# Kernel tuning notes

Measured on AMD Instinct MI355X. Metric: run time of the kernel, lower is better.

The kernel has to match this reference:

```python
import jax, jax.numpy as jnp
import numpy as np

EPS = 1e-6

def _rmsnorm(x, w):
    # Qwen3RMSNorm over last dim, computed in fp32
    var = jnp.mean(jnp.square(x), axis=-1, keepdims=True)
    return x * jax.lax.rsqrt(var + EPS) * w

def setup_inputs() -> dict:
    key = jax.random.key(0)
    ks = jax.random.split(key, 8)
    NSEQ, IN_DIM, H, G, D, SINK = 16384, 4096, 8, 4, 16, 16
    s = 0.02
    return {
        "hidden_states": jax.random.normal(ks[0], (1, NSEQ, IN_DIM), jnp.float32),
        "q_w": jax.random.normal(ks[1], (H * G * D, IN_DIM), jnp.float32) * s,
        "q_b": jax.random.normal(ks[2], (H * G * D,), jnp.float32) * s,
        "k_w": jax.random.normal(ks[3], (H * D, IN_DIM), jnp.float32) * s,
        "q_norm_w": jnp.ones((D,), jnp.float32),
        "k_norm_w": jnp.ones((D,), jnp.float32),
        "k_base": jax.random.normal(ks[4], (H, 1, SINK, D), jnp.float32) * s,
        "b": jax.random.normal(ks[5], (H, 1, G), jnp.float32) * s,
    }

def reference(hidden_states, q_w, q_b, k_w, q_norm_w, k_norm_w, k_base, b):
    H, _, SINK, D = k_base.shape
    G = b.shape[-1]
    d = jnp.sqrt(jnp.asarray(D, hidden_states.dtype))
    h = hidden_states[0]                                   # [n, in_dim]
    n = h.shape[0]
    # projections + RMSNorm
    q = _rmsnorm((h @ q_w.T + q_b).reshape(n, H, G, D), q_norm_w)   # [n,H,G,D]
    k = _rmsnorm((h @ k_w.T).reshape(n, H, D), k_norm_w)            # [n,H,D]
    # logit: per-token key against its own group queries + learned bias
    logit = jnp.einsum('nhd,nhgd->hng', k, q) / d + b               # [H,n,G]
    # logit_base: learned sink keys against queries
    logit_base = jnp.einsum('hsd,nhgd->hnsg', k_base[:, 0], q) / d  # [H,n,S,G]
    # sigmoid-difference gate, summed over sink tokens
    denom = 1.0 + jnp.sum(jnp.exp(logit_base - logit[:, :, None, :]), axis=2)  # [H,n,G]
    score = jnp.mean(1.0 / denom, axis=-1)                          # [H,n]
    return score[None]                                              # [1,H,n]
```

## Files before the change

kernel.cpp:

```cpp
#include <hip/hip_runtime.h>
#include <hip/hip_bf16.h>

typedef __attribute__((ext_vector_type(8))) short bf16x8;
typedef __attribute__((ext_vector_type(4))) float f32x4;
typedef unsigned short u16;

constexpr int NSEQ = 16384;
constexpr int KD   = 4096;
constexpr int NQ   = 512;
constexpr int NCOL = 640;
constexpr int BM   = 64;
constexpr int BK   = 64;
constexpr int NKSTEP = KD / BK;
constexpr int CHUNKS_PER_TILE = NCOL * BK * 2 / 16;
constexpr int TOTAL_CHUNKS = CHUNKS_PER_TILE * NKSTEP;

__device__ __forceinline__ unsigned bf_round(float x) {
    unsigned u = __builtin_bit_cast(unsigned, x);
    unsigned r = u + 0x7FFFu + ((u >> 16) & 1u);
    return r >> 16;
}
__device__ __forceinline__ unsigned pk2(float lo, float hi) {
    return bf_round(lo) | (bf_round(hi) << 16);
}

__global__ __launch_bounds__(256) void wconv_kernel(
    const float* __restrict__ qw, const float* __restrict__ kw,
    u16* __restrict__ Wst)
{
    int cg = blockIdx.x * 256 + threadIdx.x;
    int kk = cg / CHUNKS_PER_TILE;
    int c  = cg - kk * CHUNKS_PER_TILE;
    int n  = c >> 3;
    int s  = c & 7;
    int k0 = kk * BK + ((s ^ (n & 7)) << 3);
    const float* src = (n < NQ) ? (qw + (size_t)n * KD + k0)
                                : (kw + (size_t)(n - NQ) * KD + k0);
    float4 v0 = *(const float4*)(src);
    float4 v1 = *(const float4*)(src + 4);
    int4 o;
    o.x = (int)pk2(v0.x, v0.y);
    o.y = (int)pk2(v0.z, v0.w);
    o.z = (int)pk2(v1.x, v1.y);
    o.w = (int)pk2(v1.z, v1.w);
    *(int4*)(Wst + (size_t)cg * 8) = o;
}

__global__ __launch_bounds__(512, 2) void gemm_kernel(
    const float* __restrict__ hid, const u16* __restrict__ Wst,
    float* __restrict__ P)
{
    __shared__ char smem[NCOL * BK * 2 + BM * BK * 2];
    char* sB = smem;
    char* sA = smem + NCOL * BK * 2;

    const int t    = threadIdx.x;
    const int lane = t & 63;
    const int wid  = t >> 6;
    const int wm   = wid >> 2;
    const int wq   = wid & 3;
    const int row0 = blockIdx.x * BM;

    f32x4 acc[2][10] = {};

    const int ar = t >> 3;
    const int as = t & 7;
    const float* gA = hid + (size_t)(row0 + ar) * KD + (as << 3);
    char* aDst = sA + ar * (BK * 2) + ((as * 16) ^ ((ar & 7) << 4));

    const int bn  = lane & 15;
    const int kb8 = (lane >> 4) << 3;
    const int swz = (bn & 7) << 4;

    char* bLdsBase = sB + wid * 64 * 16;

    float4 v0 = *(const float4*)(gA);
    float4 v1 = *(const float4*)(gA + 4);

    for (int kk = 0; kk < NKSTEP; ++kk) {
        const u16* tile = Wst + (size_t)kk * (CHUNKS_PER_TILE * 8);
        #pragma unroll
        for (int it = 0; it < 10; ++it) {
            __builtin_amdgcn_global_load_lds(
                (const __attribute__((address_space(1))) void*)(tile + (size_t)(it * 512 + t) * 8),
                (__attribute__((address_space(3))) void*)(bLdsBase + it * 512 * 16),
                16, 0, 0);
        }
        int4 ap;
        ap.x = (int)pk2(v0.x, v0.y);
        ap.y = (int)pk2(v0.z, v0.w);
        ap.z = (int)pk2(v1.x, v1.y);
        ap.w = (int)pk2(v1.z, v1.w);
        *(int4*)aDst = ap;

        __syncthreads();

        if (kk + 1 < NKSTEP) {
            v0 = *(const float4*)(gA + (kk + 1) * BK);
            v1 = *(const float4*)(gA + (kk + 1) * BK + 4);
        }

        #pragma unroll
        for (int ks = 0; ks < 2; ++ks) {
            const int k2 = ks * 64 + kb8 * 2;
            const int ko = k2 ^ swz;
            bf16x8 a0 = *(const bf16x8*)(sA + (wm * 32 + bn) * 128 + ko);
            bf16x8 a1 = *(const bf16x8*)(sA + (wm * 32 + 16 + bn) * 128 + ko);
            bf16x8 bf[10];
            #pragma unroll
            for (int f = 0; f < 10; ++f) {
                const int nn = wq * 160 + f * 16 + bn;
                bf[f] = *(const bf16x8*)(sB + nn * 128 + ko);
            }
            #pragma unroll
            for (int f = 0; f < 10; ++f) {
                acc[0][f] = __builtin_amdgcn_mfma_f32_16x16x32_bf16(a0, bf[f], acc[0][f], 0, 0, 0);
                acc[1][f] = __builtin_amdgcn_mfma_f32_16x16x32_bf16(a1, bf[f], acc[1][f], 0, 0, 0);
            }
        }
        __syncthreads();
    }

    const int crow = (lane >> 4) << 2;
    const int ccol = lane & 15;
    #pragma unroll
    for (int mi = 0; mi < 2; ++mi) {
        #pragma unroll
        for (int f = 0; f < 10; ++f) {
            #pragma unroll
            for (int j = 0; j < 4; ++j) {
                int r  = row0 + wm * 32 + mi * 16 + crow + j;
                int cc = wq * 160 + f * 16 + ccol;
                P[(size_t)r * NCOL + cc] = acc[mi][f][j];
            }
        }
    }
}

__global__ __launch_bounds__(256) void gate_kernel(
    const float* __restrict__ P, const float* __restrict__ qb,
    const float* __restrict__ qnw, const float* __restrict__ knw,
    const float* __restrict__ kbase, const float* __restrict__ bb,
    float* __restrict__ out)
{
    __shared__ float skb[8 * 16 * 16];
    __shared__ float sqb[512];
    __shared__ float sb[32];
    __shared__ float snw[32];

    int tid = threadIdx.x;
    for (int i = tid; i < 2048; i += 256) skb[i] = kbase[i];
    for (int i = tid; i < 512;  i += 256) sqb[i] = qb[i];
    if (tid < 32) sb[tid] = bb[tid];
    if (tid < 16) snw[tid] = qnw[tid];
    else if (tid < 32) snw[tid] = knw[tid - 16];
    __syncthreads();

    int gid = blockIdx.x * 256 + tid;
    int tok = gid >> 5;
    int hh  = (gid >> 2) & 7;
    int g   = gid & 3;

    const float* prow = P + (size_t)tok * NCOL;
    const int qoff = (hh * 4 + g) * 16;

    float q[16];
    float ss = 0.f;
    {
        const float4* qp = (const float4*)(prow + qoff);
        const float4* bp = (const float4*)(sqb + qoff);
        #pragma unroll
        for (int i = 0; i < 4; ++i) {
            float4 v = qp[i], b4 = bp[i];
            q[4*i+0] = v.x + b4.x; q[4*i+1] = v.y + b4.y;
            q[4*i+2] = v.z + b4.z; q[4*i+3] = v.w + b4.w;
        }
        #pragma unroll
        for (int d = 0; d < 16; ++d) ss += q[d] * q[d];
    }
    float rq = rsqrtf(ss * (1.f / 16.f) + 1e-6f);
    #pragma unroll
    for (int d = 0; d < 16; ++d) q[d] *= rq * snw[d];

    float k[16];
    float sk = 0.f;
    {
        const float4* kp = (const float4*)(prow + NQ + hh * 16);
        #pragma unroll
        for (int i = 0; i < 4; ++i) {
            float4 v = kp[i];
            k[4*i+0] = v.x; k[4*i+1] = v.y; k[4*i+2] = v.z; k[4*i+3] = v.w;
        }
        #pragma unroll
        for (int d = 0; d < 16; ++d) sk += k[d] * k[d];
    }
    float rk = rsqrtf(sk * (1.f / 16.f) + 1e-6f);

    float logit = 0.f;
    #pragma unroll
    for (int d = 0; d < 16; ++d) logit += (k[d] * rk * snw[16 + d]) * q[d];
    logit = logit * 0.25f + sb[hh * 4 + g];

    float accum = 0.f;
    const float* kbh = skb + hh * 256;
    #pragma unroll
    for (int s = 0; s < 16; ++s) {
        float lb = 0.f;
        #pragma unroll
        for (int d = 0; d < 16; ++d) lb += kbh[s * 16 + d] * q[d];
        accum += __expf(lb * 0.25f - logit);
    }
    float r = 1.f / (1.f + accum);

    r += __shfl_xor(r, 1);
    r += __shfl_xor(r, 2);
    if (g == 0) out[(size_t)hh * NSEQ + tok] = r * 0.25f;
}

extern "C" void kernel_launch(void* const* d_in, const int* in_sizes, int n_in,
                              void* d_out, int out_size, void* d_ws, size_t ws_size,
                              hipStream_t stream)
{
    const float* hid = (const float*)d_in[0];
    const float* qw  = (const float*)d_in[1];
    const float* qb  = (const float*)d_in[2];
    const float* kw  = (const float*)d_in[3];
    const float* qnw = (const float*)d_in[4];
    const float* knw = (const float*)d_in[5];
    const float* kb  = (const float*)d_in[6];
    const float* bb  = (const float*)d_in[7];
    float* out = (float*)d_out;

    u16*   Wst = (u16*)d_ws;
    float* P   = (float*)((char*)d_ws + (size_t)NCOL * KD * 2);

    wconv_kernel<<<TOTAL_CHUNKS / 256, 256, 0, stream>>>(qw, kw, Wst);
    gemm_kernel<<<NSEQ / BM, 512, 0, stream>>>(hid, Wst, P);
    gate_kernel<<<NSEQ * 32 / 256, 256, 0, stream>>>(P, qb, qnw, knw, kb, bb, out);
}
```

Measured before the change: 190.7 us.

## Split-K GEMM with double-buffered LDS, larger M tile, and bf16 partial outputs

Restructures the projection GEMM into a two-way split over K, with 256 blocks of 128 rows each. Each block double-buffers LDS tiles with BK=32 and prefetches the next weight tile and A rows, so global loads overlap the MFMA work and one barrier per step is removed. The partial results are stored as bf16 into two buffers, and the gate kernel sums them, which halves the P write and read traffic per partial. In exchange the extra rounding of partials to bf16 adds precision risk, and the block count now fits only one wave of CUs.

```diff
diff --git a/kernel.cpp b/kernel.cpp
--- a/kernel.cpp
+++ b/kernel.cpp
@@ -9,11 +9,15 @@
 constexpr int KD   = 4096;
 constexpr int NQ   = 512;
 constexpr int NCOL = 640;
-constexpr int BM   = 64;
-constexpr int BK   = 64;
-constexpr int NKSTEP = KD / BK;
+constexpr int BM   = 128;
+constexpr int BK   = 32;
+constexpr int KHALF = 2048;
+constexpr int NKS  = KHALF / BK;
 constexpr int CHUNKS_PER_TILE = NCOL * BK * 2 / 16;
-constexpr int TOTAL_CHUNKS = CHUNKS_PER_TILE * NKSTEP;
+constexpr int NTILES = KD / BK;
+constexpr int TOTAL_CHUNKS = CHUNKS_PER_TILE * NTILES;
+constexpr int TILE_U16 = CHUNKS_PER_TILE * 8;
+constexpr int BUF_BYTES = 49152;
 
 __device__ __forceinline__ unsigned bf_round(float x) {
     unsigned u = __builtin_bit_cast(unsigned, x);
@@ -23,6 +27,9 @@
 __device__ __forceinline__ unsigned pk2(float lo, float hi) {
     return bf_round(lo) | (bf_round(hi) << 16);
 }
+__device__ __forceinline__ float bfu(unsigned u) {
+    return __builtin_bit_cast(float, u << 16);
+}
 
 __global__ __launch_bounds__(256) void wconv_kernel(
     const float* __restrict__ qw, const float* __restrict__ kw,
@@ -31,9 +38,9 @@
     int cg = blockIdx.x * 256 + threadIdx.x;
     int kk = cg / CHUNKS_PER_TILE;
     int c  = cg - kk * CHUNKS_PER_TILE;
-    int n  = c >> 3;
-    int s  = c & 7;
-    int k0 = kk * BK + ((s ^ (n & 7)) << 3);
+    int n  = c >> 2;
+    int s  = c & 3;
+    int k0 = kk * BK + ((s ^ (n & 3)) << 3);
     const float* src = (n < NQ) ? (qw + (size_t)n * KD + k0)
                                 : (kw + (size_t)(n - NQ) * KD + k0);
     float4 v0 = *(const float4*)(src);
@@ -48,97 +55,132 @@
 
 __global__ __launch_bounds__(512, 2) void gemm_kernel(
     const float* __restrict__ hid, const u16* __restrict__ Wst,
-    float* __restrict__ P)
-{
-    __shared__ char smem[NCOL * BK * 2 + BM * BK * 2];
-    char* sB = smem;
-    char* sA = smem + NCOL * BK * 2;
+    u16* __restrict__ P0, u16* __restrict__ P1)
+{
+    __shared__ char smem[2 * BUF_BYTES];
 
     const int t    = threadIdx.x;
     const int lane = t & 63;
     const int wid  = t >> 6;
     const int wm   = wid >> 2;
     const int wq   = wid & 3;
-    const int row0 = blockIdx.x * BM;
-
-    f32x4 acc[2][10] = {};
-
-    const int ar = t >> 3;
-    const int as = t & 7;
-    const float* gA = hid + (size_t)(row0 + ar) * KD + (as << 3);
-    char* aDst = sA + ar * (BK * 2) + ((as * 16) ^ ((ar & 7) << 4));
-
-    const int bn  = lane & 15;
-    const int kb8 = (lane >> 4) << 3;
-    const int swz = (bn & 7) << 4;
-
-    char* bLdsBase = sB + wid * 64 * 16;
-
-    float4 v0 = *(const float4*)(gA);
-    float4 v1 = *(const float4*)(gA + 4);
-
-    for (int kk = 0; kk < NKSTEP; ++kk) {
-        const u16* tile = Wst + (size_t)kk * (CHUNKS_PER_TILE * 8);
-        #pragma unroll
-        for (int it = 0; it < 10; ++it) {
+    const int mblk = blockIdx.x & 127;
+    const int kh   = blockIdx.x >> 7;
+    const int row0 = mblk * BM;
+
+    const float* hk   = hid + (size_t)row0 * KD + kh * KHALF;
+    const u16*  wbase = Wst + (size_t)(kh * NKS) * TILE_U16;
+    u16* P = kh ? P1 : P0;
+
+    f32x4 acc[4][10] = {};
+
+    const int ar  = t >> 2;
+    const int ks8 = t & 3;
+    const float* gA = hk + (size_t)ar * KD + ks8 * 8;
+    const int aWoff = ar * 64 + ((ks8 * 16) ^ ((ar & 3) << 4));
+
+    const int bn    = lane & 15;
+    const int kslot = lane >> 4;
+    const int koff  = (kslot * 16) ^ ((bn & 3) << 4);
+
+    float4 vA0a, vA0b, vA1a, vA1b;
+
+    vA0a = *(const float4*)(gA);
+    vA0b = *(const float4*)(gA + 4);
+    vA1a = *(const float4*)(gA + BK);
+    vA1b = *(const float4*)(gA + BK + 4);
+    {
+        const u16* tile = wbase;
+        #pragma unroll
+        for (int it = 0; it < 5; ++it)
             __builtin_amdgcn_global_load_lds(
                 (const __attribute__((address_space(1))) void*)(tile + (size_t)(it * 512 + t) * 8),
-                (__attribute__((address_space(3))) void*)(bLdsBase + it * 512 * 16),
+                (__attribute__((address_space(3))) void*)(smem + wid * 1024 + it * 8192),
                 16, 0, 0);
-        }
+    }
+    {
         int4 ap;
-        ap.x = (int)pk2(v0.x, v0.y);
-        ap.y = (int)pk2(v0.z, v0.w);
-        ap.z = (int)pk2(v1.x, v1.y);
-        ap.w = (int)pk2(v1.z, v1.w);
-        *(int4*)aDst = ap;
-
-        __syncthreads();
-
-        if (kk + 1 < NKSTEP) {
-            v0 = *(const float4*)(gA + (kk + 1) * BK);
-            v1 = *(const float4*)(gA + (kk + 1) * BK + 4);
-        }
-
-        #pragma unroll
-        for (int ks = 0; ks < 2; ++ks) {
-            const int k2 = ks * 64 + kb8 * 2;
-            const int ko = k2 ^ swz;
-            bf16x8 a0 = *(const bf16x8*)(sA + (wm * 32 + bn) * 128 + ko);
-            bf16x8 a1 = *(const bf16x8*)(sA + (wm * 32 + 16 + bn) * 128 + ko);
-            bf16x8 bf[10];
-            #pragma unroll
-            for (int f = 0; f < 10; ++f) {
-                const int nn = wq * 160 + f * 16 + bn;
-                bf[f] = *(const bf16x8*)(sB + nn * 128 + ko);
-            }
-            #pragma unroll
-            for (int f = 0; f < 10; ++f) {
-                acc[0][f] = __builtin_amdgcn_mfma_f32_16x16x32_bf16(a0, bf[f], acc[0][f], 0, 0, 0);
-                acc[1][f] = __builtin_amdgcn_mfma_f32_16x16x32_bf16(a1, bf[f], acc[1][f], 0, 0, 0);
-            }
-        }
-        __syncthreads();
-    }
+        ap.x = (int)pk2(vA0a.x, vA0a.y);
+        ap.y = (int)pk2(vA0a.z, vA0a.w);
+        ap.z = (int)pk2(vA0b.x, vA0b.y);
+        ap.w = (int)pk2(vA0b.z, vA0b.w);
+        *(int4*)(smem + 40960 + aWoff) = ap;
+    }
+    asm volatile("s_waitcnt lgkmcnt(0)" ::: "memory");
+    __builtin_amdgcn_s_barrier();
+
+#define GSTEP(tt, VAWa, VAWb, VALa, VALb)                                        \
+    do {                                                                         \
+        const int cur_ = (tt) & 1;                                               \
+        char* sBc = smem + cur_ * BUF_BYTES;                                     \
+        char* sAc = sBc + 40960;                                                 \
+        if ((tt) < NKS - 1) {                                                    \
+            char* sBn = smem + (cur_ ^ 1) * BUF_BYTES;                           \
+            const u16* tile = wbase + (size_t)((tt) + 1) * TILE_U16;             \
+            _Pragma("unroll")                                                    \
+            for (int it = 0; it < 5; ++it)                                       \
+                __builtin_amdgcn_global_load_lds(                                \
+                    (const __attribute__((address_space(1))) void*)(tile + (size_t)(it * 512 + t) * 8), \
+                    (__attribute__((address_space(3))) void*)(sBn + wid * 1024 + it * 8192), \
+                    16, 0, 0);                                                   \
+            {                                                                    \
+                int4 ap;                                                         \
+                ap.x = (int)pk2(VAWa.x, VAWa.y);                                 \
+                ap.y = (int)pk2(VAWa.z, VAWa.w);                                 \
+                ap.z = (int)pk2(VAWb.x, VAWb.y);                                 \
+                ap.w = (int)pk2(VAWb.z, VAWb.w);                                 \
+                *(int4*)(sBn + 40960 + aWoff) = ap;                              \
+            }                                                                    \
+            if ((tt) < NKS - 2) {                                                \
+                VALa = *(const float4*)(gA + ((tt) + 2) * BK);                   \
+                VALb = *(const float4*)(gA + ((tt) + 2) * BK + 4);               \
+                asm volatile("s_waitcnt vmcnt(7)" ::: "memory");                 \
+            } else {                                                             \
+                asm volatile("s_waitcnt vmcnt(5)" ::: "memory");                 \
+            }                                                                    \
+        } else {                                                                 \
+            asm volatile("s_waitcnt vmcnt(0)" ::: "memory");                     \
+        }                                                                        \
+        bf16x8 af[4];                                                            \
+        _Pragma("unroll")                                                        \
+        for (int m = 0; m < 4; ++m)                                              \
+            af[m] = *(const bf16x8*)(sAc + (wm * 64 + m * 16 + bn) * 64 + koff); \
+        _Pragma("unroll")                                                        \
+        for (int f = 0; f < 10; ++f) {                                           \
+            bf16x8 bfr = *(const bf16x8*)(sBc + (wq * 160 + f * 16 + bn) * 64 + koff); \
+            _Pragma("unroll")                                                    \
+            for (int m = 0; m < 4; ++m)                                          \
+                acc[m][f] = __builtin_amdgcn_mfma_f32_16x16x32_bf16(af[m], bfr, acc[m][f], 0, 0, 0); \
+        }                                                                        \
+        if ((tt) < NKS - 1) {                                                    \
+            asm volatile("s_waitcnt lgkmcnt(0)" ::: "memory");                   \
+            __builtin_amdgcn_s_barrier();                                        \
+        }                                                                        \
+    } while (0)
+
+    for (int t2 = 0; t2 < NKS / 2; ++t2) {
+        const int tt = 2 * t2;
+        GSTEP(tt,     vA1a, vA1b, vA0a, vA0b);
+        GSTEP(tt + 1, vA0a, vA0b, vA1a, vA1b);
+    }
+#undef GSTEP
 
     const int crow = (lane >> 4) << 2;
     const int ccol = lane & 15;
-    #pragma unroll
-    for (int mi = 0; mi < 2; ++mi) {
-        #pragma unroll
-        for (int f = 0; f < 10; ++f) {
+    u16* Pp = P + (size_t)(row0 + wm * 64) * NCOL + wq * 160 + ccol;
+    #pragma unroll
+    for (int m = 0; m < 4; ++m)
+        #pragma unroll
+        for (int f = 0; f < 10; ++f)
             #pragma unroll
-            for (int j = 0; j < 4; ++j) {
-                int r  = row0 + wm * 32 + mi * 16 + crow + j;
-                int cc = wq * 160 + f * 16 + ccol;
-                P[(size_t)r * NCOL + cc] = acc[mi][f][j];
-            }
-        }
-    }
+            for (int j = 0; j < 4; ++j)
+                Pp[(size_t)(m * 16 + crow + j) * NCOL + f * 16] =
+                    (u16)bf_round(acc[m][f][j]);
 }
 
 __global__ __launch_bounds__(256) void gate_kernel(
-    const float* __restrict__ P, const float* __restrict__ qb,
+    const u16* __restrict__ P0, const u16* __restrict__ P1,
+    const float* __restrict__ qb,
     const float* __restrict__ qnw, const float* __restrict__ knw,
     const float* __restrict__ kbase, const float* __restrict__ bb,
     float* __restrict__ out)
@@ -161,19 +203,26 @@
     int hh  = (gid >> 2) & 7;
     int g   = gid & 3;
 
-    const float* prow = P + (size_t)tok * NCOL;
+    const u16* r0 = P0 + (size_t)tok * NCOL;
+    const u16* r1 = P1 + (size_t)tok * NCOL;
     const int qoff = (hh * 4 + g) * 16;
 
     float q[16];
     float ss = 0.f;
     {
-        const float4* qp = (const float4*)(prow + qoff);
-        const float4* bp = (const float4*)(sqb + qoff);
-        #pragma unroll
-        for (int i = 0; i < 4; ++i) {
-            float4 v = qp[i], b4 = bp[i];
-            q[4*i+0] = v.x + b4.x; q[4*i+1] = v.y + b4.y;
-            q[4*i+2] = v.z + b4.z; q[4*i+3] = v.w + b4.w;
+        int4 a0 = *(const int4*)(r0 + qoff);
+        int4 a1 = *(const int4*)(r0 + qoff + 8);
+        int4 b0 = *(const int4*)(r1 + qoff);
+        int4 b1 = *(const int4*)(r1 + qoff + 8);
+        const int* aw = (const int*)&a0;
+        int wa[8] = {a0.x, a0.y, a0.z, a0.w, a1.x, a1.y, a1.z, a1.w};
+        int wb[8] = {b0.x, b0.y, b0.z, b0.w, b1.x, b1.y, b1.z, b1.w};
+        (void)aw;
+        #pragma unroll
+        for (int i = 0; i < 8; ++i) {
+            unsigned ua = (unsigned)wa[i], ub = (unsigned)wb[i];
+            q[2*i+0] = bfu(ua & 0xFFFFu) + bfu(ub & 0xFFFFu) + sqb[qoff + 2*i+0];
+            q[2*i+1] = bfu(ua >> 16)     + bfu(ub >> 16)     + sqb[qoff + 2*i+1];
         }
         #pragma unroll
         for (int d = 0; d < 16; ++d) ss += q[d] * q[d];
@@ -185,11 +234,18 @@
     float k[16];
     float sk = 0.f;
     {
-        const float4* kp = (const float4*)(prow + NQ + hh * 16);
-        #pragma unroll
-        for (int i = 0; i < 4; ++i) {
-            float4 v = kp[i];
-            k[4*i+0] = v.x; k[4*i+1] = v.y; k[4*i+2] = v.z; k[4*i+3] = v.w;
+        const int koffb = NQ + hh * 16;
+        int4 a0 = *(const int4*)(r0 + koffb);
+        int4 a1 = *(const int4*)(r0 + koffb + 8);
+        int4 b0 = *(const int4*)(r1 + koffb);
+        int4 b1 = *(const int4*)(r1 + koffb + 8);
+        int wa[8] = {a0.x, a0.y, a0.z, a0.w, a1.x, a1.y, a1.z, a1.w};
+        int wb[8] = {b0.x, b0.y, b0.z, b0.w, b1.x, b1.y, b1.z, b1.w};
+        #pragma unroll
+        for (int i = 0; i < 8; ++i) {
+            unsigned ua = (unsigned)wa[i], ub = (unsigned)wb[i];
+            k[2*i+0] = bfu(ua & 0xFFFFu) + bfu(ub & 0xFFFFu);
+            k[2*i+1] = bfu(ua >> 16)     + bfu(ub >> 16);
         }
         #pragma unroll
         for (int d = 0; d < 16; ++d) sk += k[d] * k[d];
@@ -231,10 +287,11 @@
     const float* bb  = (const float*)d_in[7];
     float* out = (float*)d_out;
 
-    u16*   Wst = (u16*)d_ws;
-    float* P   = (float*)((char*)d_ws + (size_t)NCOL * KD * 2);
+    u16* Wst = (u16*)d_ws;
+    u16* P0  = (u16*)((char*)d_ws + (size_t)NCOL * KD * 2);
+    u16* P1  = P0 + (size_t)NSEQ * NCOL;
 
     wconv_kernel<<<TOTAL_CHUNKS / 256, 256, 0, stream>>>(qw, kw, Wst);
-    gemm_kernel<<<NSEQ / BM, 512, 0, stream>>>(hid, Wst, P);
-    gate_kernel<<<NSEQ * 32 / 256, 256, 0, stream>>>(P, qb, qnw, knw, kb, bb, out);
-}
+    gemm_kernel<<<256, 512, 0, stream>>>(hid, Wst, P0, P1);
+    gate_kernel<<<NSEQ * 32 / 256, 256, 0, stream>>>(P0, P1, qb, qnw, knw, kb, bb, out);
+}
```

After: 186.8 us. 1.02x faster.
